# Performance work log

Hardware: AMD Instinct MI355X
Metric: run time of the kernel (lower is better)

The kernel has to match this reference:

```python
import jax, jax.numpy as jnp
import numpy as np

NUM_HEADS = 64          # also the positional-embedding size (quirk of the module)
DIM_IN, DIM_K, DIM_V = 512, 512, 64
BATCH, SEQ = 4, 1024


def setup_inputs() -> dict:
    key = jax.random.key(0)
    ks = jax.random.split(key, 7)
    s = 0.05  # weight init scale
    return {
        "x":  jax.random.normal(ks[0], (BATCH, SEQ, DIM_IN), jnp.float32),
        "Wq": jax.random.normal(ks[1], (DIM_IN, DIM_K), jnp.float32) * s,
        "bq": jax.random.normal(ks[2], (DIM_K,), jnp.float32) * s,
        "Wk": jax.random.normal(ks[3], (DIM_IN, DIM_K), jnp.float32) * s,
        "bk": jax.random.normal(ks[4], (DIM_K,), jnp.float32) * s,
        "Wv": jax.random.normal(ks[5], (DIM_IN, DIM_V), jnp.float32) * s,
        "bv": jax.random.normal(ks[6], (DIM_V,), jnp.float32) * s,
    }


def _position_embedding(n, position_size):
    # matches Position_Enbedding: cos block then sin block along feature dim
    half = position_size // 2
    pos_j = 1.0 / jnp.power(10000.0, 2.0 * jnp.arange(half, dtype=jnp.float32) / position_size)
    pos_ij = jnp.arange(n, dtype=jnp.float32)[:, None] * pos_j[None, :]   # [n, half]
    return jnp.concatenate([jnp.cos(pos_ij), jnp.sin(pos_ij)], axis=1)    # [n, position_size]


def reference(x, Wq, bq, Wk, bk, Wv, bv):
    B, n, _ = x.shape
    nh = NUM_HEADS
    dk = DIM_K // nh   # 8
    dv = DIM_V // nh   # 1
    # fused linear + ReLU, then split heads: [B, nh, n, d]
    q = jax.nn.relu(x @ Wq + bq).reshape(B, n, nh, dk).transpose(0, 2, 1, 3)
    k = jax.nn.relu(x @ Wk + bk).reshape(B, n, nh, dk).transpose(0, 2, 1, 3)
    v = jax.nn.relu(x @ Wv + bv).reshape(B, n, nh, dv).transpose(0, 2, 1, 3)
    scale = 1.0 / np.sqrt(dk).astype(np.float32)
    dist = jax.nn.softmax(jnp.einsum('bhqd,bhkd->bhqk', q, k) * scale, axis=-1)
    att = jnp.einsum('bhqk,bhkd->bhqd', dist, v)            # [B, nh, n, dv]
    att = att.transpose(0, 2, 1, 3).reshape(B, n, DIM_V)    # [B, n, dim_v]
    pe = _position_embedding(n, nh)                          # [n, nh] == [n, dim_v]
    return att + pe[None, :, :]
```

## Files before the change

kernel.cpp:

```cpp
#include <hip/hip_runtime.h>
#include <math.h>

#define BATCH 4
#define SEQ   1024
#define DIN   512
#define DKQ   512
#define DV    64
#define NH    64

typedef __attribute__((ext_vector_type(8))) short short8v;
typedef __attribute__((ext_vector_type(4))) float float4v;
typedef __attribute__((ext_vector_type(4))) unsigned int uint4v;

__device__ __forceinline__ void split_bf16(float f, unsigned short& hi, unsigned short& lo) {
    unsigned int u = __float_as_uint(f);
    hi = (unsigned short)(u >> 16);
    float l = f - __uint_as_float(u & 0xFFFF0000u);
    lo = (unsigned short)(__float_as_uint(l) >> 16);
}
__device__ __forceinline__ unsigned short f32_to_bf16_rne(float f) {
    unsigned int u = __float_as_uint(f);
    u += 0x7FFFu + ((u >> 16) & 1u);
    return (unsigned short)(u >> 16);
}
__device__ __forceinline__ float bf16_bits_to_f32(unsigned short s) {
    return __uint_as_float((unsigned int)s << 16);
}

__device__ __forceinline__ void gll16(const unsigned short* g, unsigned short* l) {
    __builtin_amdgcn_global_load_lds(
        (const __attribute__((address_space(1))) unsigned int*)(g),
        (__attribute__((address_space(3))) unsigned int*)(l),
        16, 0, 0);
}

__global__ __launch_bounds__(256)
void prepack(const float* __restrict__ x,
             const float* __restrict__ Wq, const float* __restrict__ Wk,
             const float* __restrict__ Wv,
             unsigned short* __restrict__ WhiQ, unsigned short* __restrict__ WloQ,
             unsigned short* __restrict__ WhiK, unsigned short* __restrict__ WloK,
             unsigned short* __restrict__ WhiV, unsigned short* __restrict__ WloV,
             unsigned short* __restrict__ Xhi, unsigned short* __restrict__ Xlo,
             unsigned int* __restrict__ obuf)
{
    const int z = blockIdx.z;
    const int tx = threadIdx.x, ty = threadIdx.y;
    if (z == 3) {
        const int t = ty * 32 + tx;
        const int bid = blockIdx.y * 16 + blockIdx.x;
        if (bid == 0 && t < 8)
            obuf[t] = (t < 4) ? 0x3F803F80u : 0u;
        #pragma unroll
        for (int j = 0; j < 4; ++j) {
            const int i = ((bid * 4 + j) * 256 + t) * 8;
            float4 a0 = *(const float4*)&x[i];
            float4 a1 = *(const float4*)&x[i + 4];
            float av[8] = {a0.x, a0.y, a0.z, a0.w, a1.x, a1.y, a1.z, a1.w};
            short8v h, l;
            #pragma unroll
            for (int jj = 0; jj < 8; ++jj) {
                unsigned short hh, ll; split_bf16(av[jj], hh, ll);
                h[jj] = (short)hh; l[jj] = (short)ll;
            }
            *(short8v*)&Xhi[i] = h;
            *(short8v*)&Xlo[i] = l;
        }
        return;
    }
    const int N = (z == 2) ? DV : DKQ;
    if (z == 2 && blockIdx.x >= 2) return;
    const float* __restrict__ W = (z == 0) ? Wq : (z == 1) ? Wk : Wv;
    unsigned short* __restrict__ Whi = (z == 0) ? WhiQ : (z == 1) ? WhiK : WhiV;
    unsigned short* __restrict__ Wlo = (z == 0) ? WloQ : (z == 1) ? WloK : WloV;

    __shared__ float tile[32][33];
    const int n0 = blockIdx.x * 32, k0 = blockIdx.y * 32;
    #pragma unroll
    for (int i = 0; i < 32; i += 8)
        tile[ty + i][tx] = W[(size_t)(k0 + ty + i) * N + n0 + tx];
    __syncthreads();
    #pragma unroll
    for (int i = 0; i < 32; i += 8) {
        unsigned short h, l; split_bf16(tile[tx][ty + i], h, l);
        Whi[(size_t)(n0 + ty + i) * DIN + k0 + tx] = h;
        Wlo[(size_t)(n0 + ty + i) * DIN + k0 + tx] = l;
    }
}

__global__ __launch_bounds__(512)
void proj_kernel(const unsigned short* __restrict__ Xhi,
                 const unsigned short* __restrict__ Xlo,
                 const unsigned short* __restrict__ WhiQ, const unsigned short* __restrict__ WloQ,
                 const float* __restrict__ bq,
                 const unsigned short* __restrict__ WhiK, const unsigned short* __restrict__ WloK,
                 const float* __restrict__ bk,
                 const unsigned short* __restrict__ WhiV, const unsigned short* __restrict__ WloV,
                 const float* __restrict__ bv,
                 unsigned short* __restrict__ Qpk, unsigned short* __restrict__ Kpk,
                 unsigned int* __restrict__ Vsh, unsigned int* __restrict__ Vsl)
{
    const int z = blockIdx.z;
    if (z == 2 && blockIdx.x != 0) return;
    const unsigned short* __restrict__ Whi = (z == 0) ? WhiQ : (z == 1) ? WhiK : WhiV;
    const unsigned short* __restrict__ Wlo = (z == 0) ? WloQ : (z == 1) ? WloK : WloV;
    const float* __restrict__ bias = (z == 0) ? bq : (z == 1) ? bk : bv;

    __shared__ unsigned short LDS[2][16384];

    const int t = threadIdx.x;
    const int wave = t >> 6, lane = t & 63;
    const int cl = lane & 15, g2 = lane >> 4;
    const int bm  = blockIdx.y * 128;
    const int cbb = (z == 2) ? 0 : blockIdx.x * 128;
    const int wr = wave >> 2, wc = wave & 3;
    const int NF = (z == 2) ? 1 : 2;

    const unsigned short* sAh = Xhi + (size_t)(bm + wave * 16 + cl) * DIN + g2 * 8;
    const unsigned short* sAl = Xlo + (size_t)(bm + wave * 16 + cl) * DIN + g2 * 8;
    const bool bvalid = (z != 2) || (wave < 4);
    const size_t bro = (size_t)(cbb + wave * 16 + cl) * DIN + g2 * 8;
    const unsigned short* sBh = Whi + (bvalid ? bro : 0);
    const unsigned short* sBl = Wlo + (bvalid ? bro : 0);

    auto stage = [&](int step, int bufIdx) {
        unsigned short* L = &LDS[bufIdx][0];
        const int kofs = step * 32;
        gll16(sAh + kofs, L + (wave) * 512);
        gll16(sAl + kofs, L + (wave + 8) * 512);
        if (bvalid) {
            gll16(sBh + kofs, L + (wave + 16) * 512);
            gll16(sBl + kofs, L + (wave + 24) * 512);
        }
    };

    float4v acc[4][2];
    #pragma unroll
    for (int i = 0; i < 4; ++i)
        #pragma unroll
        for (int j = 0; j < 2; ++j)
            acc[i][j] = (float4v){0.f, 0.f, 0.f, 0.f};

    stage(0, 0);
    __syncthreads();

    #pragma unroll
    for (int ks = 0; ks < 16; ++ks) {
        const int cur = ks & 1;
        if (ks < 15) stage(ks + 1, cur ^ 1);

        const unsigned short* L = &LDS[cur][0];
        short8v af_h[4], af_l[4], bf_h[2], bf_l[2];
        #pragma unroll
        for (int mt = 0; mt < 4; ++mt) {
            af_h[mt] = *(const short8v*)(L + (wr * 4 + mt) * 512 + lane * 8);
            af_l[mt] = *(const short8v*)(L + (8 + wr * 4 + mt) * 512 + lane * 8);
        }
        #pragma unroll
        for (int nf = 0; nf < 2; ++nf) {
            if (nf < NF) {
                bf_h[nf] = *(const short8v*)(L + (16 + wc * NF + nf) * 512 + lane * 8);
                bf_l[nf] = *(const short8v*)(L + (24 + wc * NF + nf) * 512 + lane * 8);
            }
        }
        #pragma unroll
        for (int mt = 0; mt < 4; ++mt)
            #pragma unroll
            for (int nf = 0; nf < 2; ++nf) {
                if (nf >= NF) continue;
                acc[mt][nf] = __builtin_amdgcn_mfma_f32_16x16x32_bf16(af_h[mt], bf_h[nf], acc[mt][nf], 0, 0, 0);
                acc[mt][nf] = __builtin_amdgcn_mfma_f32_16x16x32_bf16(af_l[mt], bf_h[nf], acc[mt][nf], 0, 0, 0);
                acc[mt][nf] = __builtin_amdgcn_mfma_f32_16x16x32_bf16(af_h[mt], bf_l[nf], acc[mt][nf], 0, 0, 0);
            }
        __syncthreads();
    }

    const float cc = 0.35355339059327373f * 1.4426950408889634f;
    if (z == 2) {
        const int n = wc * 16 + cl;
        const float bn = bias[n];
        #pragma unroll
        for (int mt = 0; mt < 4; ++mt) {
            const int row0 = bm + wr * 64 + mt * 16 + g2 * 4;
            const int bb = row0 >> 10, s0 = row0 & 1023;
            const int idx0 = (s0 >> 5) * 16 + ((s0 >> 2) & 3) * 4 + ((s0 >> 4) & 1) * 2;
            float vv[4]; unsigned short hh[4], ll[4];
            #pragma unroll
            for (int r = 0; r < 4; ++r) {
                vv[r] = fmaxf(acc[mt][0][r] + bn, 0.0f);
                hh[r] = f32_to_bf16_rne(vv[r]);
                ll[r] = f32_to_bf16_rne(vv[r] - bf16_bits_to_f32(hh[r]));
            }
            const size_t base = (size_t)((bb << 6) + n) * 512 + idx0;
            Vsh[base]     = (unsigned int)hh[0] | ((unsigned int)hh[1] << 16);
            Vsh[base + 1] = (unsigned int)hh[2] | ((unsigned int)hh[3] << 16);
            Vsl[base]     = (unsigned int)ll[0] | ((unsigned int)ll[1] << 16);
            Vsl[base + 1] = (unsigned int)ll[2] | ((unsigned int)ll[3] << 16);
        }
    } else {
        unsigned short* __restrict__ dst = (z == 0) ? Qpk : Kpk;
        #pragma unroll
        for (int nf = 0; nf < 2; ++nf) {
            const int n = cbb + wc * 32 + nf * 16 + cl;
            const float bn = bias[n];
            const int h = n >> 3, d = n & 7;
            #pragma unroll
            for (int mt = 0; mt < 4; ++mt) {
                #pragma unroll
                for (int r = 0; r < 4; ++r) {
                    const int row = bm + wr * 64 + mt * 16 + g2 * 4 + r;
                    const int bb = row >> 10, s = row & 1023;
                    float val = fmaxf(acc[mt][nf][r] + bn, 0.0f);
                    if (z == 0) val *= cc;
                    const size_t base = ((size_t)((bb << 6) + h) * SEQ + s) * 16 + d;
                    unsigned short hi = f32_to_bf16_rne(val);
                    dst[base]     = hi;
                    dst[base + 8] = f32_to_bf16_rne(val - bf16_bits_to_f32(hi));
                }
            }
        }
    }
}

__global__ __launch_bounds__(256)
void attn_kernel(const unsigned short* __restrict__ Qpk,
                 const unsigned short* __restrict__ Kpk,
                 const unsigned int* __restrict__ Vsh,
                 const unsigned int* __restrict__ Vsl,
                 const unsigned int* __restrict__ obuf,
                 float2* __restrict__ part)
{
    const int bh = blockIdx.x;
    const int yb = blockIdx.y;
    const int qhalf = yb >> 2;
    const int kq = yb & 3;
    const int t = threadIdx.x;
    const int wave = t >> 6, lane = t & 63;
    const int g = lane >> 4, cl = lane & 15;

    const unsigned short* __restrict__ qb = Qpk + (size_t)bh * SEQ * 16;
    const unsigned short* __restrict__ kb = Kpk + (size_t)bh * SEQ * 16;

    const int q0 = qhalf * 512 + wave * 128;

    short8v bq[8];
    #pragma unroll
    for (int qt = 0; qt < 8; ++qt) {
        if (g == 3) { short8v zz = {0,0,0,0,0,0,0,0}; bq[qt] = zz; }
        else bq[qt] = *(const short8v*)(qb + (size_t)(q0 + qt * 16 + cl) * 16 + ((g == 1) ? 8 : 0));
    }

    const int koff = (g >> 1) * 8;
    const unsigned short* kp = kb + kq * 4096 + cl * 16 + koff;

    const unsigned int* ap;
    int astr;
    {
        const size_t vb = (size_t)bh * 512 + kq * 128 + g * 4;
        if (cl == 0)      { ap = Vsh + vb; astr = 16; }
        else if (cl == 2) { ap = Vsl + vb; astr = 16; }
        else if (cl == 1) { ap = obuf;     astr = 0;  }
        else              { ap = obuf + 4; astr = 0;  }
    }

    const float4v c0 = {0.f, 0.f, 0.f, 0.f};
    float4v acc[8];
    #pragma unroll
    for (int qt = 0; qt < 8; ++qt) acc[qt] = c0;

    short8v k0c = *(const short8v*)kp;
    short8v k1c = *(const short8v*)(kp + 256);
    uint4v  auc = *(const uint4v*)ap;

    #pragma unroll
    for (int ss = 0; ss < 8; ++ss) {
        short8v k0n, k1n; uint4v aun;
        if (ss < 7) {
            k0n = *(const short8v*)(kp + 512);
            k1n = *(const short8v*)(kp + 768);
            aun = *(const uint4v*)(ap + astr);
        }
        kp += 512; ap += astr;
        const short8v af = __builtin_bit_cast(short8v, auc);
        #pragma unroll
        for (int qt = 0; qt < 8; ++qt) {
            float4v s0 = __builtin_amdgcn_mfma_f32_16x16x32_bf16(k0c, bq[qt], c0, 0, 0, 0);
            float4v s1 = __builtin_amdgcn_mfma_f32_16x16x32_bf16(k1c, bq[qt], c0, 0, 0, 0);
            float p00 = __builtin_amdgcn_exp2f(s0[0]);
            float p01 = __builtin_amdgcn_exp2f(s0[1]);
            float p02 = __builtin_amdgcn_exp2f(s0[2]);
            float p03 = __builtin_amdgcn_exp2f(s0[3]);
            float p10 = __builtin_amdgcn_exp2f(s1[0]);
            float p11 = __builtin_amdgcn_exp2f(s1[1]);
            float p12 = __builtin_amdgcn_exp2f(s1[2]);
            float p13 = __builtin_amdgcn_exp2f(s1[3]);
            unsigned int pk0 = __builtin_amdgcn_perm(__float_as_uint(p01), __float_as_uint(p00), 0x07060302u);
            unsigned int pk1 = __builtin_amdgcn_perm(__float_as_uint(p03), __float_as_uint(p02), 0x07060302u);
            unsigned int pk2 = __builtin_amdgcn_perm(__float_as_uint(p11), __float_as_uint(p10), 0x07060302u);
            unsigned int pk3 = __builtin_amdgcn_perm(__float_as_uint(p13), __float_as_uint(p12), 0x07060302u);
            uint4v pu = {pk0, pk1, pk2, pk3};
            acc[qt] = __builtin_amdgcn_mfma_f32_16x16x32_bf16(af, __builtin_bit_cast(short8v, pu), acc[qt], 0, 0, 0);
        }
        if (ss < 7) { k0c = k0n; k1c = k1n; auc = aun; }
    }

    if (g == 0) {
        #pragma unroll
        for (int qt = 0; qt < 8; ++qt) {
            const int row = q0 + qt * 16 + cl;
            float2 pr;
            pr.x = acc[qt][0] + acc[qt][2];
            pr.y = acc[qt][1];
            part[(size_t)(kq * 256 + bh) * SEQ + row] = pr;
        }
    }
}

__global__ __launch_bounds__(256)
void merge_kernel(const float2* __restrict__ part, float* __restrict__ out)
{
    const int tid = blockIdx.x * 256 + threadIdx.x;
    const int h = tid & 63;
    const int q = (tid >> 6) & 1023;
    const int b = tid >> 16;
    const int bh = (b << 6) + h;
    float num = 0.f, den = 0.f;
    #pragma unroll
    for (int kq = 0; kq < 4; ++kq) {
        float2 p = part[(size_t)(kq * 256 + bh) * SEQ + q];
        num += p.x; den += p.y;
    }
    const float fr = __builtin_amdgcn_exp2f((float)(h & 31) * -0.4152410118609203f);
    const float pe = (h < 32) ? cosf((float)q * fr) : sinf((float)q * fr);
    out[tid] = num / den + pe;
}

extern "C" void kernel_launch(void* const* d_in, const int* in_sizes, int n_in,
                              void* d_out, int out_size, void* d_ws, size_t ws_size,
                              hipStream_t stream)
{
    const float* x  = (const float*)d_in[0];
    const float* Wq = (const float*)d_in[1];
    const float* bq = (const float*)d_in[2];
    const float* Wk = (const float*)d_in[3];
    const float* bk = (const float*)d_in[4];
    const float* Wv = (const float*)d_in[5];
    const float* bv = (const float*)d_in[6];
    float* out = (float*)d_out;

    unsigned short* Qpk = (unsigned short*)d_ws;
    unsigned short* Kpk = Qpk + (size_t)BATCH * NH * SEQ * 16;
    unsigned int* Vsh = (unsigned int*)(Kpk + (size_t)BATCH * NH * SEQ * 16);
    unsigned int* Vsl = Vsh + (size_t)BATCH * NH * (SEQ / 2);
    unsigned int* obuf = Vsl + (size_t)BATCH * NH * (SEQ / 2);
    unsigned short* Xhi = (unsigned short*)(obuf + 64);
    unsigned short* Xlo = Xhi + (size_t)BATCH * SEQ * DIN;
    float2* part = (float2*)Xhi;
    unsigned short* WhiQ = Xlo + (size_t)BATCH * SEQ * DIN;
    unsigned short* WloQ = WhiQ + (size_t)DIN * DKQ;
    unsigned short* WhiK = WloQ + (size_t)DIN * DKQ;
    unsigned short* WloK = WhiK + (size_t)DIN * DKQ;
    unsigned short* WhiV = WloK + (size_t)DIN * DKQ;
    unsigned short* WloV = WhiV + (size_t)DIN * DV;

    prepack<<<dim3(16, 16, 4), dim3(32, 8), 0, stream>>>(
        x, Wq, Wk, Wv, WhiQ, WloQ, WhiK, WloK, WhiV, WloV, Xhi, Xlo, obuf);
    proj_kernel<<<dim3(4, 32, 3), 512, 0, stream>>>(
        Xhi, Xlo, WhiQ, WloQ, bq, WhiK, WloK, bk, WhiV, WloV, bv, Qpk, Kpk, Vsh, Vsl);
    attn_kernel<<<dim3(256, 8), 256, 0, stream>>>(Qpk, Kpk, Vsh, Vsl, obuf, part);
    merge_kernel<<<dim3((BATCH * SEQ * DV) / 256), 256, 0, stream>>>(part, out);
}
```

Baseline: 86.35 us.

## Split projection into Q/K and V kernels with full-K LDS-resident X tiles

Replaces the single 3-way projection GEMM with a Q/K kernel and a separate V kernel. Each block stages a 32-row X slice (hi and lo planes, all of K) into LDS once, then streams weight fragments straight from global memory into registers with double buffering, so there are no per-K-step barriers. This removes the idle z==2 blocks of the old grid and gives more, smaller blocks. The cost is redundant weight reads from global/L2 per block. The attention kernel also gets an occupancy hint in its launch bounds.

```diff
diff --git a/kernel.cpp b/kernel.cpp
--- a/kernel.cpp
+++ b/kernel.cpp
@@ -89,140 +89,197 @@
 }
 
 __global__ __launch_bounds__(512)
-void proj_kernel(const unsigned short* __restrict__ Xhi,
-                 const unsigned short* __restrict__ Xlo,
-                 const unsigned short* __restrict__ WhiQ, const unsigned short* __restrict__ WloQ,
-                 const float* __restrict__ bq,
-                 const unsigned short* __restrict__ WhiK, const unsigned short* __restrict__ WloK,
-                 const float* __restrict__ bk,
-                 const unsigned short* __restrict__ WhiV, const unsigned short* __restrict__ WloV,
-                 const float* __restrict__ bv,
-                 unsigned short* __restrict__ Qpk, unsigned short* __restrict__ Kpk,
-                 unsigned int* __restrict__ Vsh, unsigned int* __restrict__ Vsl)
-{
-    const int z = blockIdx.z;
-    if (z == 2 && blockIdx.x != 0) return;
-    const unsigned short* __restrict__ Whi = (z == 0) ? WhiQ : (z == 1) ? WhiK : WhiV;
-    const unsigned short* __restrict__ Wlo = (z == 0) ? WloQ : (z == 1) ? WloK : WloV;
-    const float* __restrict__ bias = (z == 0) ? bq : (z == 1) ? bk : bv;
-
-    __shared__ unsigned short LDS[2][16384];
+void qk_kernel(const unsigned short* __restrict__ Xhi,
+               const unsigned short* __restrict__ Xlo,
+               const unsigned short* __restrict__ WhiQ, const unsigned short* __restrict__ WloQ,
+               const float* __restrict__ bq,
+               const unsigned short* __restrict__ WhiK, const unsigned short* __restrict__ WloK,
+               const float* __restrict__ bk,
+               unsigned short* __restrict__ Qpk, unsigned short* __restrict__ Kpk)
+{
+    const int zq = blockIdx.x;
+    const unsigned short* __restrict__ Whi = zq ? WhiK : WhiQ;
+    const unsigned short* __restrict__ Wlo = zq ? WloK : WloQ;
+    const float* __restrict__ bias = zq ? bk : bq;
+    unsigned short* __restrict__ dst = zq ? Kpk : Qpk;
+
+    __shared__ unsigned short LDS[32768];
 
     const int t = threadIdx.x;
     const int wave = t >> 6, lane = t & 63;
     const int cl = lane & 15, g2 = lane >> 4;
-    const int bm  = blockIdx.y * 128;
-    const int cbb = (z == 2) ? 0 : blockIdx.x * 128;
-    const int wr = wave >> 2, wc = wave & 3;
-    const int NF = (z == 2) ? 1 : 2;
-
-    const unsigned short* sAh = Xhi + (size_t)(bm + wave * 16 + cl) * DIN + g2 * 8;
-    const unsigned short* sAl = Xlo + (size_t)(bm + wave * 16 + cl) * DIN + g2 * 8;
-    const bool bvalid = (z != 2) || (wave < 4);
-    const size_t bro = (size_t)(cbb + wave * 16 + cl) * DIN + g2 * 8;
-    const unsigned short* sBh = Whi + (bvalid ? bro : 0);
-    const unsigned short* sBl = Wlo + (bvalid ? bro : 0);
-
-    auto stage = [&](int step, int bufIdx) {
-        unsigned short* L = &LDS[bufIdx][0];
-        const int kofs = step * 32;
-        gll16(sAh + kofs, L + (wave) * 512);
-        gll16(sAl + kofs, L + (wave + 8) * 512);
-        if (bvalid) {
-            gll16(sBh + kofs, L + (wave + 16) * 512);
-            gll16(sBl + kofs, L + (wave + 24) * 512);
-        }
-    };
-
-    float4v acc[4][2];
-    #pragma unroll
-    for (int i = 0; i < 4; ++i)
-        #pragma unroll
-        for (int j = 0; j < 2; ++j)
+    const int bm = blockIdx.y * 32;
+
+    #pragma unroll
+    for (int j = 0; j < 8; ++j) {
+        const int chunk = wave * 8 + j;
+        const int ks = chunk >> 2, plane = (chunk >> 1) & 1, mt = chunk & 1;
+        const unsigned short* src = (plane ? Xlo : Xhi)
+            + (size_t)(bm + mt * 16 + cl) * DIN + ks * 32 + g2 * 8;
+        gll16(src, &LDS[chunk * 512]);
+    }
+    __syncthreads();
+
+    const unsigned short* pBh = Whi + (size_t)(wave * 64 + cl) * DIN + g2 * 8;
+    const unsigned short* pBl = Wlo + (size_t)(wave * 64 + cl) * DIN + g2 * 8;
+
+    float4v acc[2][4];
+    #pragma unroll
+    for (int i = 0; i < 2; ++i)
+        #pragma unroll
+        for (int j = 0; j < 4; ++j)
             acc[i][j] = (float4v){0.f, 0.f, 0.f, 0.f};
 
-    stage(0, 0);
-    __syncthreads();
-
-    #pragma unroll
-    for (int ks = 0; ks < 16; ++ks) {
-        const int cur = ks & 1;
-        if (ks < 15) stage(ks + 1, cur ^ 1);
-
-        const unsigned short* L = &LDS[cur][0];
-        short8v af_h[4], af_l[4], bf_h[2], bf_l[2];
-        #pragma unroll
-        for (int mt = 0; mt < 4; ++mt) {
-            af_h[mt] = *(const short8v*)(L + (wr * 4 + mt) * 512 + lane * 8);
-            af_l[mt] = *(const short8v*)(L + (8 + wr * 4 + mt) * 512 + lane * 8);
-        }
-        #pragma unroll
-        for (int nf = 0; nf < 2; ++nf) {
-            if (nf < NF) {
-                bf_h[nf] = *(const short8v*)(L + (16 + wc * NF + nf) * 512 + lane * 8);
-                bf_l[nf] = *(const short8v*)(L + (24 + wc * NF + nf) * 512 + lane * 8);
-            }
-        }
-        #pragma unroll
-        for (int mt = 0; mt < 4; ++mt)
-            #pragma unroll
-            for (int nf = 0; nf < 2; ++nf) {
-                if (nf >= NF) continue;
-                acc[mt][nf] = __builtin_amdgcn_mfma_f32_16x16x32_bf16(af_h[mt], bf_h[nf], acc[mt][nf], 0, 0, 0);
-                acc[mt][nf] = __builtin_amdgcn_mfma_f32_16x16x32_bf16(af_l[mt], bf_h[nf], acc[mt][nf], 0, 0, 0);
-                acc[mt][nf] = __builtin_amdgcn_mfma_f32_16x16x32_bf16(af_h[mt], bf_l[nf], acc[mt][nf], 0, 0, 0);
-            }
-        __syncthreads();
-    }
+    short8v B0h[4], B0l[4], B1h[4], B1l[4];
+
+#define LOADB(KS, BH, BL)                                                     \
+    _Pragma("unroll")                                                         \
+    for (int nf = 0; nf < 4; ++nf) {                                          \
+        BH[nf] = *(const short8v*)(pBh + nf * (16 * DIN) + (KS) * 32);        \
+        BL[nf] = *(const short8v*)(pBl + nf * (16 * DIN) + (KS) * 32);        \
+    }
+
+#define STEP(KS, BH, BL)                                                      \
+    {                                                                         \
+        short8v ah[2], al[2];                                                 \
+        _Pragma("unroll")                                                     \
+        for (int mt = 0; mt < 2; ++mt) {                                      \
+            ah[mt] = *(const short8v*)&LDS[((KS) * 4 + mt) * 512 + lane * 8]; \
+            al[mt] = *(const short8v*)&LDS[((KS) * 4 + 2 + mt) * 512 + lane * 8]; \
+        }                                                                     \
+        _Pragma("unroll")                                                     \
+        for (int mt = 0; mt < 2; ++mt)                                        \
+            _Pragma("unroll")                                                 \
+            for (int nf = 0; nf < 4; ++nf) {                                  \
+                acc[mt][nf] = __builtin_amdgcn_mfma_f32_16x16x32_bf16(ah[mt], BH[nf], acc[mt][nf], 0, 0, 0); \
+                acc[mt][nf] = __builtin_amdgcn_mfma_f32_16x16x32_bf16(al[mt], BH[nf], acc[mt][nf], 0, 0, 0); \
+                acc[mt][nf] = __builtin_amdgcn_mfma_f32_16x16x32_bf16(ah[mt], BL[nf], acc[mt][nf], 0, 0, 0); \
+            }                                                                 \
+    }
+
+    LOADB(0, B0h, B0l);
+    #pragma unroll
+    for (int kp2 = 0; kp2 < 8; ++kp2) {
+        const int ks0 = kp2 * 2;
+        LOADB(ks0 + 1, B1h, B1l);
+        STEP(ks0, B0h, B0l);
+        if (ks0 + 2 < 16) { LOADB(ks0 + 2, B0h, B0l); }
+        STEP(ks0 + 1, B1h, B1l);
+    }
+#undef LOADB
+#undef STEP
 
     const float cc = 0.35355339059327373f * 1.4426950408889634f;
-    if (z == 2) {
-        const int n = wc * 16 + cl;
+    #pragma unroll
+    for (int nf = 0; nf < 4; ++nf) {
+        const int n = wave * 64 + nf * 16 + cl;
         const float bn = bias[n];
-        #pragma unroll
-        for (int mt = 0; mt < 4; ++mt) {
-            const int row0 = bm + wr * 64 + mt * 16 + g2 * 4;
-            const int bb = row0 >> 10, s0 = row0 & 1023;
-            const int idx0 = (s0 >> 5) * 16 + ((s0 >> 2) & 3) * 4 + ((s0 >> 4) & 1) * 2;
-            float vv[4]; unsigned short hh[4], ll[4];
+        const int h = n >> 3, d = n & 7;
+        #pragma unroll
+        for (int mt = 0; mt < 2; ++mt) {
             #pragma unroll
             for (int r = 0; r < 4; ++r) {
-                vv[r] = fmaxf(acc[mt][0][r] + bn, 0.0f);
-                hh[r] = f32_to_bf16_rne(vv[r]);
-                ll[r] = f32_to_bf16_rne(vv[r] - bf16_bits_to_f32(hh[r]));
+                const int row = bm + mt * 16 + g2 * 4 + r;
+                const int bb = row >> 10, s = row & 1023;
+                float val = fmaxf(acc[mt][nf][r] + bn, 0.0f);
+                if (zq == 0) val *= cc;
+                const size_t base = ((size_t)((bb << 6) + h) * SEQ + s) * 16 + d;
+                unsigned short hi = f32_to_bf16_rne(val);
+                dst[base]     = hi;
+                dst[base + 8] = f32_to_bf16_rne(val - bf16_bits_to_f32(hi));
             }
-            const size_t base = (size_t)((bb << 6) + n) * 512 + idx0;
-            Vsh[base]     = (unsigned int)hh[0] | ((unsigned int)hh[1] << 16);
-            Vsh[base + 1] = (unsigned int)hh[2] | ((unsigned int)hh[3] << 16);
-            Vsl[base]     = (unsigned int)ll[0] | ((unsigned int)ll[1] << 16);
-            Vsl[base + 1] = (unsigned int)ll[2] | ((unsigned int)ll[3] << 16);
-        }
-    } else {
-        unsigned short* __restrict__ dst = (z == 0) ? Qpk : Kpk;
-        #pragma unroll
-        for (int nf = 0; nf < 2; ++nf) {
-            const int n = cbb + wc * 32 + nf * 16 + cl;
-            const float bn = bias[n];
-            const int h = n >> 3, d = n & 7;
-            #pragma unroll
-            for (int mt = 0; mt < 4; ++mt) {
-                #pragma unroll
-                for (int r = 0; r < 4; ++r) {
-                    const int row = bm + wr * 64 + mt * 16 + g2 * 4 + r;
-                    const int bb = row >> 10, s = row & 1023;
-                    float val = fmaxf(acc[mt][nf][r] + bn, 0.0f);
-                    if (z == 0) val *= cc;
-                    const size_t base = ((size_t)((bb << 6) + h) * SEQ + s) * 16 + d;
-                    unsigned short hi = f32_to_bf16_rne(val);
-                    dst[base]     = hi;
-                    dst[base + 8] = f32_to_bf16_rne(val - bf16_bits_to_f32(hi));
-                }
-            }
         }
     }
 }
 
 __global__ __launch_bounds__(256)
+void v_kernel(const unsigned short* __restrict__ Xhi,
+              const unsigned short* __restrict__ Xlo,
+              const unsigned short* __restrict__ WhiV, const unsigned short* __restrict__ WloV,
+              const float* __restrict__ bv,
+              unsigned int* __restrict__ Vsh, unsigned int* __restrict__ Vsl)
+{
+    __shared__ unsigned short LDS[32768];
+
+    const int t = threadIdx.x;
+    const int wave = t >> 6, lane = t & 63;
+    const int cl = lane & 15, g2 = lane >> 4;
+    const int bm = blockIdx.x * 32;
+
+    #pragma unroll
+    for (int j = 0; j < 16; ++j) {
+        const int chunk = wave * 16 + j;
+        const int ks = chunk >> 2, plane = (chunk >> 1) & 1, mt = chunk & 1;
+        const unsigned short* src = (plane ? Xlo : Xhi)
+            + (size_t)(bm + mt * 16 + cl) * DIN + ks * 32 + g2 * 8;
+        gll16(src, &LDS[chunk * 512]);
+    }
+    __syncthreads();
+
+    const unsigned short* pBh = WhiV + (size_t)(wave * 16 + cl) * DIN + g2 * 8;
+    const unsigned short* pBl = WloV + (size_t)(wave * 16 + cl) * DIN + g2 * 8;
+
+    float4v acc[2];
+    acc[0] = (float4v){0.f, 0.f, 0.f, 0.f};
+    acc[1] = (float4v){0.f, 0.f, 0.f, 0.f};
+
+    short8v B0h, B0l, B1h, B1l;
+
+#define VLOADB(KS, BH, BL)                                   \
+    BH = *(const short8v*)(pBh + (KS) * 32);                 \
+    BL = *(const short8v*)(pBl + (KS) * 32);
+
+#define VSTEP(KS, BH, BL)                                                     \
+    {                                                                         \
+        short8v ah[2], al[2];                                                 \
+        _Pragma("unroll")                                                     \
+        for (int mt = 0; mt < 2; ++mt) {                                      \
+            ah[mt] = *(const short8v*)&LDS[((KS) * 4 + mt) * 512 + lane * 8]; \
+            al[mt] = *(const short8v*)&LDS[((KS) * 4 + 2 + mt) * 512 + lane * 8]; \
+        }                                                                     \
+        _Pragma("unroll")                                                     \
+        for (int mt = 0; mt < 2; ++mt) {                                      \
+            acc[mt] = __builtin_amdgcn_mfma_f32_16x16x32_bf16(ah[mt], BH, acc[mt], 0, 0, 0); \
+            acc[mt] = __builtin_amdgcn_mfma_f32_16x16x32_bf16(al[mt], BH, acc[mt], 0, 0, 0); \
+            acc[mt] = __builtin_amdgcn_mfma_f32_16x16x32_bf16(ah[mt], BL, acc[mt], 0, 0, 0); \
+        }                                                                     \
+    }
+
+    VLOADB(0, B0h, B0l);
+    #pragma unroll
+    for (int kp2 = 0; kp2 < 8; ++kp2) {
+        const int ks0 = kp2 * 2;
+        VLOADB(ks0 + 1, B1h, B1l);
+        VSTEP(ks0, B0h, B0l);
+        if (ks0 + 2 < 16) { VLOADB(ks0 + 2, B0h, B0l); }
+        VSTEP(ks0 + 1, B1h, B1l);
+    }
+#undef VLOADB
+#undef VSTEP
+
+    const int n = wave * 16 + cl;
+    const float bn = bv[n];
+    #pragma unroll
+    for (int mt = 0; mt < 2; ++mt) {
+        const int row0 = bm + mt * 16 + g2 * 4;
+        const int bb = row0 >> 10, s0 = row0 & 1023;
+        const int idx0 = (s0 >> 5) * 16 + ((s0 >> 2) & 3) * 4 + ((s0 >> 4) & 1) * 2;
+        float vv[4]; unsigned short hh[4], ll[4];
+        #pragma unroll
+        for (int r = 0; r < 4; ++r) {
+            vv[r] = fmaxf(acc[mt][r] + bn, 0.0f);
+            hh[r] = f32_to_bf16_rne(vv[r]);
+            ll[r] = f32_to_bf16_rne(vv[r] - bf16_bits_to_f32(hh[r]));
+        }
+        const size_t base = (size_t)((bb << 6) + n) * 512 + idx0;
+        Vsh[base]     = (unsigned int)hh[0] | ((unsigned int)hh[1] << 16);
+        Vsh[base + 1] = (unsigned int)hh[2] | ((unsigned int)hh[3] << 16);
+        Vsl[base]     = (unsigned int)ll[0] | ((unsigned int)ll[1] << 16);
+        Vsl[base + 1] = (unsigned int)ll[2] | ((unsigned int)ll[3] << 16);
+    }
+}
+
+__global__ __launch_bounds__(256, 4)
 void attn_kernel(const unsigned short* __restrict__ Qpk,
                  const unsigned short* __restrict__ Kpk,
                  const unsigned int* __restrict__ Vsh,
@@ -365,8 +422,10 @@
 
     prepack<<<dim3(16, 16, 4), dim3(32, 8), 0, stream>>>(
         x, Wq, Wk, Wv, WhiQ, WloQ, WhiK, WloK, WhiV, WloV, Xhi, Xlo, obuf);
-    proj_kernel<<<dim3(4, 32, 3), 512, 0, stream>>>(
-        Xhi, Xlo, WhiQ, WloQ, bq, WhiK, WloK, bk, WhiV, WloV, bv, Qpk, Kpk, Vsh, Vsl);
+    qk_kernel<<<dim3(2, 128), 512, 0, stream>>>(
+        Xhi, Xlo, WhiQ, WloQ, bq, WhiK, WloK, bk, Qpk, Kpk);
+    v_kernel<<<dim3(128), 256, 0, stream>>>(
+        Xhi, Xlo, WhiV, WloV, bv, Vsh, Vsl);
     attn_kernel<<<dim3(256, 8), 256, 0, stream>>>(Qpk, Kpk, Vsh, Vsl, obuf, part);
     merge_kernel<<<dim3((BATCH * SEQ * DV) / 256), 256, 0, stream>>>(part, out);
 }
```

New measurement: 101.5 us. 17.6% more time.
